# Kernel tuning notes

Hardware: AMD Instinct MI355X
Metric: run time of the kernel (lower is better)

The kernel has to match this reference:

```python
import jax, jax.numpy as jnp
import numpy as np

CHAN = 256
KEY_DIM = 64
VALUE_DIM = 64
HEADS = 8


def _conv1x1(x, W, b):
    # x: [b,c,h,w], W: [out,c], b: [out]  (1x1 conv == channel matmul)
    return jnp.einsum('bchw,oc->bohw', x, W) + b[None, :, None, None]


def setup_inputs() -> dict:
    key = jax.random.key(0)
    ks = jax.random.split(key, 9)
    qk_out = KEY_DIM * HEADS
    v_out = VALUE_DIM * HEADS
    s_in = 1.0 / np.sqrt(CHAN)
    s_out = 1.0 / np.sqrt(v_out)
    return {
        'x': jax.random.normal(ks[0], (16, CHAN, 64, 64), dtype=jnp.float32),
        'Wq': jax.random.uniform(ks[1], (qk_out, CHAN), jnp.float32, -s_in, s_in),
        'bq': jax.random.uniform(ks[2], (qk_out,), jnp.float32, -s_in, s_in),
        'Wk': jax.random.uniform(ks[3], (qk_out, CHAN), jnp.float32, -s_in, s_in),
        'bk': jax.random.uniform(ks[4], (qk_out,), jnp.float32, -s_in, s_in),
        'Wv': jax.random.uniform(ks[5], (v_out, CHAN), jnp.float32, -s_in, s_in),
        'bv': jax.random.uniform(ks[6], (v_out,), jnp.float32, -s_in, s_in),
        'Wo': jax.random.uniform(ks[7], (CHAN, v_out), jnp.float32, -s_out, s_out),
        'bo': jax.random.uniform(ks[8], (CHAN,), jnp.float32, -s_out, s_out),
    }


def reference(x, Wq, bq, Wk, bk, Wv, bv, Wo, bo):
    b, c, h, w = x.shape
    n = h * w
    scale = KEY_DIM ** (-0.25)
    q = _conv1x1(x, Wq, bq).reshape(b, HEADS, KEY_DIM, n) * scale
    k = _conv1x1(x, Wk, bk).reshape(b, HEADS, KEY_DIM, n) * scale
    v = _conv1x1(x, Wv, bv).reshape(b, HEADS, VALUE_DIM, n)
    k = jax.nn.softmax(k, axis=-1)       # over positions n
    q = jax.nn.softmax(q, axis=-2)       # over key_dim d (norm_queries=True)
    ctx = jnp.einsum('bhdn,bhen->bhde', k, v)   # [b,h,d,e] small context
    out = jnp.einsum('bhdn,bhde->bhen', q, ctx) # [b,h,e,n]
    out = out.reshape(b, HEADS * VALUE_DIM, h, w)
    return _conv1x1(out, Wo, bo)
```

## Files before the change

kernel.cpp:

```cpp
#include <hip/hip_runtime.h>
#include <hip/hip_bf16.h>

typedef unsigned short u16;
typedef unsigned int u32;
typedef __attribute__((ext_vector_type(8))) short bf16x8;
typedef __attribute__((ext_vector_type(4))) float f32x4;

#define NB 16
#define NPOS 4096
#define QK_SCALE 0.35355339059327373f

__device__ __forceinline__ float bf2f(u32 u) {
  union { u32 i; float f; } x; x.i = u << 16; return x.f;
}
__device__ __forceinline__ u16 f2bf(float f) {
  union { float f; u32 i; } x; x.f = f;
  u32 r = x.i + 0x7fffu + ((x.i >> 16) & 1u);
  return (u16)(r >> 16);
}

__device__ __forceinline__ void async16(u16* ldst, const u16* gsrc) {
  __builtin_amdgcn_global_load_lds(
      (const __attribute__((address_space(1))) unsigned int*)gsrc,
      (__attribute__((address_space(3))) unsigned int*)ldst, 16, 0, 0);
}

__global__ __launch_bounds__(256) void transpose_x(const float* __restrict__ x,
                                                   u16* __restrict__ xT) {
  int b = blockIdx.z;
  int c0 = blockIdx.y * 64;
  int n0 = blockIdx.x * 64;
  const float* xp = x + ((long)b * 256 + c0) * 4096 + n0;
  u16* op = xT + ((long)b * 4096 + n0) * 256 + c0;
  __shared__ float T[64][65];
  int t = threadIdx.x;
  {
    int cl = t >> 2, nc = (t & 3) * 16;
    #pragma unroll
    for (int u = 0; u < 4; ++u) {
      float4 v = *(const float4*)&xp[(long)cl * 4096 + nc + u * 4];
      T[nc + u*4 + 0][cl] = v.x; T[nc + u*4 + 1][cl] = v.y;
      T[nc + u*4 + 2][cl] = v.z; T[nc + u*4 + 3][cl] = v.w;
    }
  }
  __syncthreads();
  {
    int nl = t >> 2, cc = (t & 3) * 16;
    u32 wv[8];
    #pragma unroll
    for (int j = 0; j < 8; ++j)
      wv[j] = (u32)f2bf(T[nl][cc + 2*j]) | ((u32)f2bf(T[nl][cc + 2*j + 1]) << 16);
    *(uint4*)&op[(long)nl * 256 + cc]     = make_uint4(wv[0], wv[1], wv[2], wv[3]);
    *(uint4*)&op[(long)nl * 256 + cc + 8] = make_uint4(wv[4], wv[5], wv[6], wv[7]);
  }
}

__global__ __launch_bounds__(256) void convert_wqkv(
    const float* __restrict__ Wq, const float* __restrict__ Wk, const float* __restrict__ Wv,
    const float* __restrict__ bq, const float* __restrict__ bk, const float* __restrict__ bv,
    u16* __restrict__ W, float* __restrict__ bias)
{
  if (blockIdx.x < 96) {
    int gid = blockIdx.x * 256 + threadIdx.x;
    int which = gid >> 13;
    int off = (gid & 8191) * 16;
    const float* src = which == 0 ? Wq : which == 1 ? Wk : Wv;
    float scl = which == 2 ? 1.0f : QK_SCALE;
    u16* dst = W + which * 131072;
    u32 wv_[8];
    #pragma unroll
    for (int u = 0; u < 4; ++u) {
      float4 a = *(const float4*)&src[off + u * 4];
      wv_[u*2+0] = (u32)f2bf(a.x*scl) | ((u32)f2bf(a.y*scl) << 16);
      wv_[u*2+1] = (u32)f2bf(a.z*scl) | ((u32)f2bf(a.w*scl) << 16);
    }
    *(uint4*)&dst[off]     = make_uint4(wv_[0], wv_[1], wv_[2], wv_[3]);
    *(uint4*)&dst[off + 8] = make_uint4(wv_[4], wv_[5], wv_[6], wv_[7]);
  } else {
    int t = threadIdx.x;
    #pragma unroll
    for (int u = 0; u < 6; ++u) {
      int i = t * 6 + u;
      if (i < 1536) {
        int which = i >> 9, r = i & 511;
        float v = which == 0 ? bq[r] : which == 1 ? bk[r] : bv[r];
        bias[i] = which == 2 ? v : v * QK_SCALE;
      }
    }
  }
}

__global__ __launch_bounds__(256) void proj_qkv(
    const u16* __restrict__ W, const float* __restrict__ bias,
    const u16* __restrict__ xT, u16* __restrict__ qT,
    u16* __restrict__ kx, u16* __restrict__ vb)
{
  int b = blockIdx.z;
  const u16* Bm = xT + (long)b * (4096L * 256);
  int mb = blockIdx.y;
  int m0 = mb * 128, n0 = blockIdx.x * 128;

  __shared__ u16 sm[32768];
  int t = threadIdx.x, w = t >> 6, l = t & 63;
  int lr = l & 15, lk = l >> 4;
  int wr = w >> 1, wcq = w & 1;
  int srow8 = l >> 3;
  int ksl = ((l & 7) ^ srow8) * 8;

  f32x4 acc[4][4];
  #pragma unroll
  for (int i = 0; i < 4; ++i)
    #pragma unroll
    for (int j = 0; j < 4; ++j) acc[i][j] = (f32x4){0.f, 0.f, 0.f, 0.f};

#define STAGE_P(buf, kt) { \
    u16* base_ = sm + (buf) * 16384; \
    int k0_ = (kt) * 64; \
    _Pragma("unroll") \
    for (int i_ = 0; i_ < 4; ++i_) { \
      int seg_ = w * 4 + i_; \
      int row_ = seg_ * 8 + srow8; \
      async16(base_ + seg_ * 512, W + (long)(m0 + row_) * 256 + k0_ + ksl); \
      async16(base_ + 8192 + seg_ * 512, Bm + (long)(n0 + row_) * 256 + k0_ + ksl); \
    } }

#define COMPUTE_P(buf) { \
    const u16* base_ = sm + (buf) * 16384; \
    _Pragma("unroll") \
    for (int s_ = 0; s_ < 2; ++s_) { \
      bf16x8 af_[4], bf_[4]; \
      _Pragma("unroll") \
      for (int mi_ = 0; mi_ < 4; ++mi_) { \
        int row_ = wr * 64 + mi_ * 16 + lr; \
        int slot_ = (s_ * 4 + lk) ^ (row_ & 7); \
        af_[mi_] = *(const bf16x8*)&base_[row_ * 64 + slot_ * 8]; \
      } \
      _Pragma("unroll") \
      for (int ni_ = 0; ni_ < 4; ++ni_) { \
        int row_ = wcq * 64 + ni_ * 16 + lr; \
        int slot_ = (s_ * 4 + lk) ^ (row_ & 7); \
        bf_[ni_] = *(const bf16x8*)&base_[8192 + row_ * 64 + slot_ * 8]; \
      } \
      _Pragma("unroll") \
      for (int mi_ = 0; mi_ < 4; ++mi_) \
        _Pragma("unroll") \
        for (int ni_ = 0; ni_ < 4; ++ni_) \
          acc[mi_][ni_] = __builtin_amdgcn_mfma_f32_16x16x32_bf16(af_[mi_], bf_[ni_], acc[mi_][ni_], 0, 0, 0); \
    } }

#define WAITBAR asm volatile("s_waitcnt vmcnt(0)" ::: "memory"); __builtin_amdgcn_s_barrier();

  STAGE_P(0, 0)
  WAITBAR
  STAGE_P(1, 1)
  COMPUTE_P(0)
  WAITBAR
  STAGE_P(0, 2)
  COMPUTE_P(1)
  WAITBAR
  STAGE_P(1, 3)
  COMPUTE_P(0)
  WAITBAR
  COMPUTE_P(1)

  int mbase = m0 + wr * 64;
  int nbase = n0 + wcq * 64;

  if (mb < 4) {
    float bv_[4][4];
    #pragma unroll
    for (int mi = 0; mi < 4; ++mi)
      #pragma unroll
      for (int r = 0; r < 4; ++r) bv_[mi][r] = bias[mbase + mi * 16 + lk * 4 + r];
    u16* qp = qT + (long)b * (4096L * 512);
    #pragma unroll
    for (int ni = 0; ni < 4; ++ni) {
      float ssum = 0.f;
      #pragma unroll
      for (int mi = 0; mi < 4; ++mi)
        #pragma unroll
        for (int r = 0; r < 4; ++r) {
          float e = __expf(acc[mi][ni][r] + bv_[mi][r]);
          acc[mi][ni][r] = e; ssum += e;
        }
      ssum += __shfl_xor(ssum, 16);
      ssum += __shfl_xor(ssum, 32);
      float inv = 1.f / ssum;
      int n = nbase + ni * 16 + lr;
      #pragma unroll
      for (int mi = 0; mi < 4; ++mi) {
        ushort4 o;
        o.x = f2bf(acc[mi][ni][0] * inv); o.y = f2bf(acc[mi][ni][1] * inv);
        o.z = f2bf(acc[mi][ni][2] * inv); o.w = f2bf(acc[mi][ni][3] * inv);
        *(ushort4*)&qp[(long)n * 512 + mbase + mi * 16 + lk * 4] = o;
      }
    }
  } else if (mb < 8) {
    u16* kp = kx + (long)b * (512L * 4096) + (long)(mbase - 512) * 4096;
    #pragma unroll
    for (int mi = 0; mi < 4; ++mi)
      #pragma unroll
      for (int r = 0; r < 4; ++r) {
        int mr = mi * 16 + lk * 4 + r;
        float bi = bias[mbase + mr];
        #pragma unroll
        for (int ni = 0; ni < 4; ++ni) {
          int n = nbase + ni * 16 + lr;
          kp[(long)mr * 4096 + n] = f2bf(__expf(acc[mi][ni][r] + bi));
        }
      }
  } else {
    u16* vp = vb + (long)b * (512L * 4096) + (long)(mbase - 1024) * 4096;
    #pragma unroll
    for (int mi = 0; mi < 4; ++mi)
      #pragma unroll
      for (int r = 0; r < 4; ++r) {
        int mr = mi * 16 + lk * 4 + r;
        float bi = bias[mbase + mr];
        #pragma unroll
        for (int ni = 0; ni < 4; ++ni) {
          int n = nbase + ni * 16 + lr;
          vp[(long)mr * 4096 + n] = f2bf(acc[mi][ni][r] + bi);
        }
      }
  }
#undef STAGE_P
#undef COMPUTE_P
}

__global__ __launch_bounds__(64) void ctx_mfma(
    const u16* __restrict__ kx, const u16* __restrict__ vv,
    float* __restrict__ Sp, float* __restrict__ Zp)
{
  int ns = blockIdx.x;
  int bh = blockIdx.y;
  const u16* kp = kx + (long)bh * 64 * NPOS + ns * 256;
  const u16* vp = vv + (long)bh * 64 * NPOS + ns * 256;
  int l = threadIdx.x, lr = l & 15, lk = l >> 4;
  f32x4 acc[4][4]; f32x4 az[4];
  #pragma unroll
  for (int i = 0; i < 4; ++i) {
    az[i] = (f32x4){0.f, 0.f, 0.f, 0.f};
    #pragma unroll
    for (int j = 0; j < 4; ++j) acc[i][j] = (f32x4){0.f, 0.f, 0.f, 0.f};
  }
  bf16x8 ones;
  #pragma unroll
  for (int j = 0; j < 8; ++j) ones[j] = (short)0x3F80;

  #pragma unroll 2
  for (int s = 0; s < 8; ++s) {
    int nn = s * 32 + lk * 8;
    bf16x8 a[4], bb[4];
    #pragma unroll
    for (int mi = 0; mi < 4; ++mi)
      a[mi] = *(const bf16x8*)(kp + (long)(mi * 16 + lr) * NPOS + nn);
    #pragma unroll
    for (int ni = 0; ni < 4; ++ni)
      bb[ni] = *(const bf16x8*)(vp + (long)(ni * 16 + lr) * NPOS + nn);
    #pragma unroll
    for (int mi = 0; mi < 4; ++mi)
      az[mi] = __builtin_amdgcn_mfma_f32_16x16x32_bf16(a[mi], ones, az[mi], 0, 0, 0);
    #pragma unroll
    for (int mi = 0; mi < 4; ++mi)
      #pragma unroll
      for (int ni = 0; ni < 4; ++ni)
        acc[mi][ni] = __builtin_amdgcn_mfma_f32_16x16x32_bf16(a[mi], bb[ni], acc[mi][ni], 0, 0, 0);
  }
  float* sp = Sp + ((long)ns * 128 + bh) * 4096;
  #pragma unroll
  for (int mi = 0; mi < 4; ++mi)
    #pragma unroll
    for (int ni = 0; ni < 4; ++ni)
      #pragma unroll
      for (int r = 0; r < 4; ++r)
        sp[(mi * 16 + lk * 4 + r) * 64 + ni * 16 + lr] = acc[mi][ni][r];
  if (lr == 0) {
    float* zp = Zp + ((long)ns * 128 + bh) * 64;
    #pragma unroll
    for (int mi = 0; mi < 4; ++mi)
      #pragma unroll
      for (int r = 0; r < 4; ++r)
        zp[mi * 16 + lk * 4 + r] = az[mi][r];
  }
}

__global__ __launch_bounds__(256) void wc_kernel(
    const float* __restrict__ Sp, const float* __restrict__ Zp,
    const float* __restrict__ Wo, u16* __restrict__ Wc)
{
  int bh = blockIdx.x;
  int bb = bh >> 3, h = bh & 7;
  __shared__ float Cs[64][65];
  __shared__ float Ws[64][65];
  int tid = threadIdx.x, tx = tid & 15, ty = tid >> 4;

  {
    int row = tid >> 2;
    int ec  = (tid & 3) << 4;
    float Zr = 0.f;
    #pragma unroll
    for (int si = 0; si < 16; ++si) Zr += Zp[((long)si * 128 + bh) * 64 + row];
    float invZ = 1.f / Zr;
    #pragma unroll
    for (int u = 0; u < 4; ++u) {
      float4 s = make_float4(0, 0, 0, 0);
      #pragma unroll
      for (int si = 0; si < 16; ++si) {
        float4 tv = *(const float4*)&Sp[(((long)si * 128 + bh) * 64 + row) * 64 + ec + u * 4];
        s.x += tv.x; s.y += tv.y; s.z += tv.z; s.w += tv.w;
      }
      Cs[row][ec + u*4 + 0] = s.x * invZ; Cs[row][ec + u*4 + 1] = s.y * invZ;
      Cs[row][ec + u*4 + 2] = s.z * invZ; Cs[row][ec + u*4 + 3] = s.w * invZ;
    }
  }
  for (int cc = 0; cc < 4; ++cc) {
    __syncthreads();
    {
      int row = tid >> 2;
      int ec  = (tid & 3) << 4;
      #pragma unroll
      for (int u = 0; u < 4; ++u) {
        float4 wv = *(const float4*)&Wo[(long)(cc * 64 + row) * 512 + h * 64 + ec + u * 4];
        Ws[row][ec + u*4 + 0] = wv.x; Ws[row][ec + u*4 + 1] = wv.y;
        Ws[row][ec + u*4 + 2] = wv.z; Ws[row][ec + u*4 + 3] = wv.w;
      }
    }
    __syncthreads();
    float acc[4][4] = {};
    #pragma unroll 8
    for (int e = 0; e < 64; ++e) {
      float a[4], b[4];
      #pragma unroll
      for (int i = 0; i < 4; ++i) a[i] = Ws[(ty << 2) + i][e];
      #pragma unroll
      for (int j = 0; j < 4; ++j) b[j] = Cs[(tx << 2) + j][e];
      #pragma unroll
      for (int i = 0; i < 4; ++i)
        #pragma unroll
        for (int j = 0; j < 4; ++j)
          acc[i][j] += a[i] * b[j];
    }
    #pragma unroll
    for (int i = 0; i < 4; ++i) {
      int co = cc * 64 + (ty << 2) + i;
      ushort4 o;
      o.x = f2bf(acc[i][0]); o.y = f2bf(acc[i][1]);
      o.z = f2bf(acc[i][2]); o.w = f2bf(acc[i][3]);
      *(ushort4*)&Wc[((long)bb * 256 + co) * 512 + h * 64 + (tx << 2)] = o;
    }
  }
}

__global__ __launch_bounds__(256) void final_gemm(
    const u16* __restrict__ Wc, const u16* __restrict__ qTg,
    const float* __restrict__ bo, float* __restrict__ out)
{
  int b = blockIdx.z;
  const u16* A = Wc + (long)b * (256L * 512);
  const u16* Bm = qTg + (long)b * (4096L * 512);
  int m0 = blockIdx.y * 128, n0 = blockIdx.x * 128;

  __shared__ u16 sm[32768];
  int t = threadIdx.x, w = t >> 6, l = t & 63;
  int lr = l & 15, lk = l >> 4;
  int wr = w >> 1, wcq = w & 1;
  int srow8 = l >> 3;
  int ksl = ((l & 7) ^ srow8) * 8;

  f32x4 acc[4][4];
  #pragma unroll
  for (int i = 0; i < 4; ++i)
    #pragma unroll
    for (int j = 0; j < 4; ++j) acc[i][j] = (f32x4){0.f, 0.f, 0.f, 0.f};

#define STAGE_F(buf, kt) { \
    u16* base_ = sm + (buf) * 16384; \
    int k0_ = (kt) * 64; \
    _Pragma("unroll") \
    for (int i_ = 0; i_ < 4; ++i_) { \
      int seg_ = w * 4 + i_; \
      int row_ = seg_ * 8 + srow8; \
      async16(base_ + seg_ * 512, A + (long)(m0 + row_) * 512 + k0_ + ksl); \
      async16(base_ + 8192 + seg_ * 512, Bm + (long)(n0 + row_) * 512 + k0_ + ksl); \
    } }

#define COMPUTE_F(buf) { \
    const u16* base_ = sm + (buf) * 16384; \
    _Pragma("unroll") \
    for (int s_ = 0; s_ < 2; ++s_) { \
      bf16x8 af_[4], bf_[4]; \
      _Pragma("unroll") \
      for (int mi_ = 0; mi_ < 4; ++mi_) { \
        int row_ = wr * 64 + mi_ * 16 + lr; \
        int slot_ = (s_ * 4 + lk) ^ (row_ & 7); \
        af_[mi_] = *(const bf16x8*)&base_[row_ * 64 + slot_ * 8]; \
      } \
      _Pragma("unroll") \
      for (int ni_ = 0; ni_ < 4; ++ni_) { \
        int row_ = wcq * 64 + ni_ * 16 + lr; \
        int slot_ = (s_ * 4 + lk) ^ (row_ & 7); \
        bf_[ni_] = *(const bf16x8*)&base_[8192 + row_ * 64 + slot_ * 8]; \
      } \
      _Pragma("unroll") \
      for (int mi_ = 0; mi_ < 4; ++mi_) \
        _Pragma("unroll") \
        for (int ni_ = 0; ni_ < 4; ++ni_) \
          acc[mi_][ni_] = __builtin_amdgcn_mfma_f32_16x16x32_bf16(af_[mi_], bf_[ni_], acc[mi_][ni_], 0, 0, 0); \
    } }

  STAGE_F(0, 0)
  WAITBAR
  #pragma unroll
  for (int kt = 0; kt < 8; ++kt) {
    if (kt < 7) {
      if ((kt & 1) == 0) { STAGE_F(1, kt + 1) } else { STAGE_F(0, kt + 1) }
    }
    if ((kt & 1) == 0) { COMPUTE_F(0) } else { COMPUTE_F(1) }
    if (kt < 7) { WAITBAR }
  }

  float* op = out + (long)b * (256L * 4096);
  int mbase = m0 + wr * 64;
  int nbase = n0 + wcq * 64;
  #pragma unroll
  for (int mi = 0; mi < 4; ++mi)
    #pragma unroll
    for (int r = 0; r < 4; ++r) {
      int m = mbase + mi * 16 + lk * 4 + r;
      float bi = bo[m];
      #pragma unroll
      for (int ni = 0; ni < 4; ++ni) {
        int n = nbase + ni * 16 + lr;
        op[(long)m * 4096 + n] = acc[mi][ni][r] + bi;
      }
    }
#undef STAGE_F
#undef COMPUTE_F
}

extern "C" void kernel_launch(void* const* d_in, const int* in_sizes, int n_in,
                              void* d_out, int out_size, void* d_ws, size_t ws_size,
                              hipStream_t stream) {
  (void)in_sizes; (void)n_in; (void)out_size; (void)ws_size;
  const float* x  = (const float*)d_in[0];
  const float* Wq = (const float*)d_in[1];
  const float* bq = (const float*)d_in[2];
  const float* Wk = (const float*)d_in[3];
  const float* bk = (const float*)d_in[4];
  const float* Wv = (const float*)d_in[5];
  const float* bv = (const float*)d_in[6];
  const float* Wo = (const float*)d_in[7];
  const float* bo = (const float*)d_in[8];
  float* out = (float*)d_out;

  char* ws = (char*)d_ws;
  u16*   xT    = (u16*)(ws);
  float* Sp    = (float*)(ws);
  u16*   qT    = (u16*)(ws + 33554432L);
  u16*   kx    = (u16*)(ws + 100663296L);
  u16*   Wcb   = (u16*)(ws + 167772160L);
  u16*   Wqkvb = (u16*)(ws + 171966464L);
  float* bqkv  = (float*)(ws + 172752896L);
  float* Zp    = (float*)(ws + 172759040L);
  u16*   vb    = (u16*)d_out;

  dim3 blk(256);
  hipLaunchKernelGGL(transpose_x, dim3(64, 4, NB), blk, 0, stream, x, xT);
  hipLaunchKernelGGL(convert_wqkv, dim3(97), blk, 0, stream, Wq, Wk, Wv, bq, bk, bv, Wqkvb, bqkv);
  hipLaunchKernelGGL(proj_qkv, dim3(32, 12, NB), blk, 0, stream, Wqkvb, bqkv, xT, qT, kx, vb);
  hipLaunchKernelGGL(ctx_mfma, dim3(16, 128), dim3(64), 0, stream, kx, vb, Sp, Zp);
  hipLaunchKernelGGL(wc_kernel, dim3(128), blk, 0, stream, Sp, Zp, Wo, Wcb);
  hipLaunchKernelGGL(final_gemm, dim3(32, 2, NB), blk, 0, stream, Wcb, qT, bo, out);
}
```

Baseline: 306.2 us.

## Deepen GEMM prefetch pipelines and swap MFMA operands for vectorized row stores

The projection and final GEMMs now keep two stages in flight and wait with vmcnt(8) instead of draining all loads before each barrier. MFMA operands are swapped for the K/V projection and the final GEMM so each lane holds four consecutive positions, which allows ushort4/float4 row stores in place of scalar strided stores. The projection is split into two template instantiations, one for Q and one for K/V, to remove the branch. The ctx kernel double-buffers its register loads. The partial vmcnt waits depend on the exact count of outstanding loads per stage, so a wrong count could race.

```diff
diff --git a/kernel.cpp b/kernel.cpp
--- a/kernel.cpp
+++ b/kernel.cpp
@@ -24,6 +24,10 @@
       (const __attribute__((address_space(1))) unsigned int*)gsrc,
       (__attribute__((address_space(3))) unsigned int*)ldst, 16, 0, 0);
 }
+
+#define VW8 asm volatile("s_waitcnt vmcnt(8)" ::: "memory");
+#define VW0 asm volatile("s_waitcnt vmcnt(0)" ::: "memory");
+#define BAR __builtin_amdgcn_s_barrier();
 
 __global__ __launch_bounds__(256) void transpose_x(const float* __restrict__ x,
                                                    u16* __restrict__ xT) {
@@ -90,7 +94,8 @@
   }
 }
 
-__global__ __launch_bounds__(256) void proj_qkv(
+template<int MODE>
+__global__ __launch_bounds__(256) void proj_kern(
     const u16* __restrict__ W, const float* __restrict__ bias,
     const u16* __restrict__ xT, u16* __restrict__ qT,
     u16* __restrict__ kx, u16* __restrict__ vb)
@@ -98,7 +103,8 @@
   int b = blockIdx.z;
   const u16* Bm = xT + (long)b * (4096L * 256);
   int mb = blockIdx.y;
-  int m0 = mb * 128, n0 = blockIdx.x * 128;
+  int m0 = (MODE == 0 ? 0 : 512) + mb * 128;
+  int n0 = blockIdx.x * 128;
 
   __shared__ u16 sm[32768];
   int t = threadIdx.x, w = t >> 6, l = t & 63;
@@ -145,28 +151,30 @@
       for (int mi_ = 0; mi_ < 4; ++mi_) \
         _Pragma("unroll") \
         for (int ni_ = 0; ni_ < 4; ++ni_) \
-          acc[mi_][ni_] = __builtin_amdgcn_mfma_f32_16x16x32_bf16(af_[mi_], bf_[ni_], acc[mi_][ni_], 0, 0, 0); \
+          acc[mi_][ni_] = MODE == 0 \
+            ? __builtin_amdgcn_mfma_f32_16x16x32_bf16(af_[mi_], bf_[ni_], acc[mi_][ni_], 0, 0, 0) \
+            : __builtin_amdgcn_mfma_f32_16x16x32_bf16(bf_[ni_], af_[mi_], acc[mi_][ni_], 0, 0, 0); \
     } }
 
-#define WAITBAR asm volatile("s_waitcnt vmcnt(0)" ::: "memory"); __builtin_amdgcn_s_barrier();
-
   STAGE_P(0, 0)
-  WAITBAR
   STAGE_P(1, 1)
+  VW8 BAR
   COMPUTE_P(0)
-  WAITBAR
+  BAR
   STAGE_P(0, 2)
+  VW8 BAR
   COMPUTE_P(1)
-  WAITBAR
+  BAR
   STAGE_P(1, 3)
+  VW8 BAR
   COMPUTE_P(0)
-  WAITBAR
+  BAR
+  VW0 BAR
   COMPUTE_P(1)
 
-  int mbase = m0 + wr * 64;
-  int nbase = n0 + wcq * 64;
-
-  if (mb < 4) {
+  if (MODE == 0) {
+    int mbase = m0 + wr * 64;
+    int nbase = n0 + wcq * 64;
     float bv_[4][4];
     #pragma unroll
     for (int mi = 0; mi < 4; ++mi)
@@ -195,34 +203,30 @@
         *(ushort4*)&qp[(long)n * 512 + mbase + mi * 16 + lk * 4] = o;
       }
     }
-  } else if (mb < 8) {
-    u16* kp = kx + (long)b * (512L * 4096) + (long)(mbase - 512) * 4096;
-    #pragma unroll
-    for (int mi = 0; mi < 4; ++mi)
-      #pragma unroll
-      for (int r = 0; r < 4; ++r) {
-        int mr = mi * 16 + lk * 4 + r;
-        float bi = bias[mbase + mr];
-        #pragma unroll
-        for (int ni = 0; ni < 4; ++ni) {
-          int n = nbase + ni * 16 + lr;
-          kp[(long)mr * 4096 + n] = f2bf(__expf(acc[mi][ni][r] + bi));
+  } else {
+    bool is_k = (mb < 4);
+    u16* dst = is_k ? (kx + (long)b * (512L * 4096) - 512L * 4096)
+                    : (vb + (long)b * (512L * 4096) - 1024L * 4096);
+    #pragma unroll
+    for (int mi = 0; mi < 4; ++mi) {
+      int m = m0 + wr * 64 + mi * 16 + lr;
+      float bi = bias[m];
+      u16* rowp = dst + (long)m * 4096;
+      #pragma unroll
+      for (int ni = 0; ni < 4; ++ni) {
+        int nb2 = n0 + wcq * 64 + ni * 16 + lk * 4;
+        f32x4 v = acc[mi][ni];
+        ushort4 o;
+        if (is_k) {
+          o.x = f2bf(__expf(v[0] + bi)); o.y = f2bf(__expf(v[1] + bi));
+          o.z = f2bf(__expf(v[2] + bi)); o.w = f2bf(__expf(v[3] + bi));
+        } else {
+          o.x = f2bf(v[0] + bi); o.y = f2bf(v[1] + bi);
+          o.z = f2bf(v[2] + bi); o.w = f2bf(v[3] + bi);
         }
+        *(ushort4*)&rowp[nb2] = o;
       }
-  } else {
-    u16* vp = vb + (long)b * (512L * 4096) + (long)(mbase - 1024) * 4096;
-    #pragma unroll
-    for (int mi = 0; mi < 4; ++mi)
-      #pragma unroll
-      for (int r = 0; r < 4; ++r) {
-        int mr = mi * 16 + lk * 4 + r;
-        float bi = bias[mbase + mr];
-        #pragma unroll
-        for (int ni = 0; ni < 4; ++ni) {
-          int n = nbase + ni * 16 + lr;
-          vp[(long)mr * 4096 + n] = f2bf(acc[mi][ni][r] + bi);
-        }
-      }
+    }
   }
 #undef STAGE_P
 #undef COMPUTE_P
@@ -248,25 +252,37 @@
   #pragma unroll
   for (int j = 0; j < 8; ++j) ones[j] = (short)0x3F80;
 
-  #pragma unroll 2
-  for (int s = 0; s < 8; ++s) {
-    int nn = s * 32 + lk * 8;
-    bf16x8 a[4], bb[4];
-    #pragma unroll
-    for (int mi = 0; mi < 4; ++mi)
-      a[mi] = *(const bf16x8*)(kp + (long)(mi * 16 + lr) * NPOS + nn);
-    #pragma unroll
-    for (int ni = 0; ni < 4; ++ni)
-      bb[ni] = *(const bf16x8*)(vp + (long)(ni * 16 + lr) * NPOS + nn);
-    #pragma unroll
-    for (int mi = 0; mi < 4; ++mi)
-      az[mi] = __builtin_amdgcn_mfma_f32_16x16x32_bf16(a[mi], ones, az[mi], 0, 0, 0);
-    #pragma unroll
-    for (int mi = 0; mi < 4; ++mi)
-      #pragma unroll
-      for (int ni = 0; ni < 4; ++ni)
-        acc[mi][ni] = __builtin_amdgcn_mfma_f32_16x16x32_bf16(a[mi], bb[ni], acc[mi][ni], 0, 0, 0);
-  }
+#define CTX_LOAD(as, bs, s) { \
+    int nn_ = (s) * 32 + lk * 8; \
+    _Pragma("unroll") \
+    for (int mi_ = 0; mi_ < 4; ++mi_) \
+      as[mi_] = *(const bf16x8*)(kp + (long)(mi_ * 16 + lr) * NPOS + nn_); \
+    _Pragma("unroll") \
+    for (int ni_ = 0; ni_ < 4; ++ni_) \
+      bs[ni_] = *(const bf16x8*)(vp + (long)(ni_ * 16 + lr) * NPOS + nn_); }
+
+#define CTX_MF(as, bs) { \
+    _Pragma("unroll") \
+    for (int mi_ = 0; mi_ < 4; ++mi_) \
+      az[mi_] = __builtin_amdgcn_mfma_f32_16x16x32_bf16(as[mi_], ones, az[mi_], 0, 0, 0); \
+    _Pragma("unroll") \
+    for (int mi_ = 0; mi_ < 4; ++mi_) \
+      _Pragma("unroll") \
+      for (int ni_ = 0; ni_ < 4; ++ni_) \
+        acc[mi_][ni_] = __builtin_amdgcn_mfma_f32_16x16x32_bf16(as[mi_], bs[ni_], acc[mi_][ni_], 0, 0, 0); }
+
+  bf16x8 a0[4], b0[4], a1[4], b1[4];
+  CTX_LOAD(a0, b0, 0)
+  #pragma unroll
+  for (int s = 0; s < 8; s += 2) {
+    if (s + 1 < 8) CTX_LOAD(a1, b1, s + 1)
+    CTX_MF(a0, b0)
+    if (s + 2 < 8) CTX_LOAD(a0, b0, s + 2)
+    if (s + 1 < 8) CTX_MF(a1, b1)
+  }
+#undef CTX_LOAD
+#undef CTX_MF
+
   float* sp = Sp + ((long)ns * 128 + bh) * 4096;
   #pragma unroll
   for (int mi = 0; mi < 4; ++mi)
@@ -406,35 +422,37 @@
       for (int mi_ = 0; mi_ < 4; ++mi_) \
         _Pragma("unroll") \
         for (int ni_ = 0; ni_ < 4; ++ni_) \
-          acc[mi_][ni_] = __builtin_amdgcn_mfma_f32_16x16x32_bf16(af_[mi_], bf_[ni_], acc[mi_][ni_], 0, 0, 0); \
+          acc[mi_][ni_] = __builtin_amdgcn_mfma_f32_16x16x32_bf16(bf_[ni_], af_[mi_], acc[mi_][ni_], 0, 0, 0); \
     } }
 
   STAGE_F(0, 0)
-  WAITBAR
+  STAGE_F(1, 1)
+  VW8 BAR
   #pragma unroll
   for (int kt = 0; kt < 8; ++kt) {
-    if (kt < 7) {
-      if ((kt & 1) == 0) { STAGE_F(1, kt + 1) } else { STAGE_F(0, kt + 1) }
-    }
     if ((kt & 1) == 0) { COMPUTE_F(0) } else { COMPUTE_F(1) }
-    if (kt < 7) { WAITBAR }
+    BAR
+    if (kt < 6) {
+      if ((kt & 1) == 0) { STAGE_F(0, kt + 2) } else { STAGE_F(1, kt + 2) }
+      VW8 BAR
+    } else if (kt == 6) {
+      VW0 BAR
+    }
   }
 
   float* op = out + (long)b * (256L * 4096);
-  int mbase = m0 + wr * 64;
-  int nbase = n0 + wcq * 64;
-  #pragma unroll
-  for (int mi = 0; mi < 4; ++mi)
-    #pragma unroll
-    for (int r = 0; r < 4; ++r) {
-      int m = mbase + mi * 16 + lk * 4 + r;
-      float bi = bo[m];
-      #pragma unroll
-      for (int ni = 0; ni < 4; ++ni) {
-        int n = nbase + ni * 16 + lr;
-        op[(long)m * 4096 + n] = acc[mi][ni][r] + bi;
-      }
-    }
+  #pragma unroll
+  for (int mi = 0; mi < 4; ++mi) {
+    int m = m0 + wr * 64 + mi * 16 + lr;
+    float bi = bo[m];
+    float* rowp = op + (long)m * 4096;
+    #pragma unroll
+    for (int ni = 0; ni < 4; ++ni) {
+      int nb2 = n0 + wcq * 64 + ni * 16 + lk * 4;
+      f32x4 v = acc[mi][ni];
+      *(float4*)&rowp[nb2] = make_float4(v[0] + bi, v[1] + bi, v[2] + bi, v[3] + bi);
+    }
+  }
 #undef STAGE_F
 #undef COMPUTE_F
 }
@@ -468,7 +486,10 @@
   dim3 blk(256);
   hipLaunchKernelGGL(transpose_x, dim3(64, 4, NB), blk, 0, stream, x, xT);
   hipLaunchKernelGGL(convert_wqkv, dim3(97), blk, 0, stream, Wq, Wk, Wv, bq, bk, bv, Wqkvb, bqkv);
-  hipLaunchKernelGGL(proj_qkv, dim3(32, 12, NB), blk, 0, stream, Wqkvb, bqkv, xT, qT, kx, vb);
+  hipLaunchKernelGGL(HIP_KERNEL_NAME(proj_kern<0>), dim3(32, 4, NB), blk, 0, stream,
+                     Wqkvb, bqkv, xT, qT, kx, vb);
+  hipLaunchKernelGGL(HIP_KERNEL_NAME(proj_kern<1>), dim3(32, 8, NB), blk, 0, stream,
+                     Wqkvb, bqkv, xT, qT, kx, vb);
   hipLaunchKernelGGL(ctx_mfma, dim3(16, 128), dim3(64), 0, stream, kx, vb, Sp, Zp);
   hipLaunchKernelGGL(wc_kernel, dim3(128), blk, 0, stream, Sp, Zp, Wo, Wcb);
   hipLaunchKernelGGL(final_gemm, dim3(32, 2, NB), blk, 0, stream, Wcb, qT, bo, out);
```

Measured after the change: 299.7 us. -2.1%, faster.
